# Kernel optimization log

Measured on AMD Instinct MI355X. Metric: run time of the kernel, lower is better.

Reference implementation:

```python
import jax, jax.numpy as jnp
import numpy as np

R = 8            # ring rank
N = 4            # num cores
D_IN = 2048
D_OUT = 2048
LIN = [512, 512, 512, 512]   # local input dims (additive split)
LOUT = [512, 512, 512, 512]  # local output dims (additive split)


def setup_inputs() -> dict:
    key = jax.random.key(0)
    ks = jax.random.split(key, 6)
    inp = {"inputs": jax.random.normal(ks[0], (4, 1024, D_IN), dtype=jnp.float32)}
    for i in range(N):
        lf = LOUT[i] * LIN[i]
        std = np.sqrt(2.0 / (R + lf)).astype(np.float32)
        inp[f"core{i}"] = jax.random.normal(ks[1 + i], (R, lf, R), dtype=jnp.float32) * std
    inp["bias"] = jnp.zeros((D_OUT,), dtype=jnp.float32)
    return inp


def reference(inputs, core0, core1, core2, core3, bias):
    cores = [core0, core1, core2, core3]
    batch_shape = inputs.shape[:-1]
    x = inputs.reshape(-1, D_IN)                      # [B, D_IN]
    B = x.shape[0]

    # split input additively across cores
    offs = np.cumsum([0] + LIN)
    xs = [x[:, offs[i]:offs[i + 1]] for i in range(N)]  # each [B, d_in_i]
    Gs = [cores[i].reshape(R, LOUT[i], LIN[i], R) for i in range(N)]

    # environment messages: S_i[b,r,s] = sum_{o,x} G_i[r,o,x,s] * x_i[b,x]
    S = [jnp.einsum('roxs,bx->brs', Gs[i], xs[i]) for i in range(N)]

    eye = jnp.broadcast_to(jnp.eye(R, dtype=x.dtype), (B, R, R))
    # prefix P_i = S_0 ... S_{i-1}, suffix Q_i = S_{i+1} ... S_{N-1}
    P = [eye]
    for i in range(1, N):
        P.append(jnp.matmul(P[-1], S[i - 1]))
    Q = [eye]
    for i in range(N - 2, -1, -1):
        Q.append(jnp.matmul(S[i + 1], Q[-1]))
    Q = Q[::-1]

    outs = []
    for i in range(N):
        # Env_i[b,r,s] = sum_p Q_i[b,s,p] P_i[b,p,r]  (trace closure of the ring)
        env = jnp.einsum('bsp,bpr->brs', Q[i], P[i])
        # M_i[b,r,o,s] = sum_x G_i[r,o,x,s] x_i[b,x]
        M = jnp.einsum('roxs,bx->bros', Gs[i], xs[i])
        outs.append(jnp.einsum('brs,bros->bo', env, M))
    out = jnp.concatenate(outs, axis=-1) + bias       # [B, D_OUT]
    return out.reshape(batch_shape + (D_OUT,))
```

## Files before the change

### kernel.cpp

```cpp
#include <hip/hip_runtime.h>
#include <stdint.h>

#define B_TOT   4096
#define D_IN    2048
#define D_OUT   2048
#define NCHUNK  4
#define LIN     512
#define LOUT    512
#define RK      8
#define CORE_R_STRIDE 2097152
#define CORE_O_STRIDE 4096

#define WS_XT    0
#define WS_GHAT  8388608
#define WS_S     (8388608 + 131072)
#define WS_ENVT  (8388608 + 131072 + 1048576)

typedef __attribute__((ext_vector_type(8))) __bf16 bf16x8;
typedef __attribute__((ext_vector_type(4))) float f32x4;
typedef __attribute__((ext_vector_type(4))) unsigned int u32x4;

__global__ __launch_bounds__(256) void k_transpose(const float* __restrict__ x,
                                                   float* __restrict__ xT) {
    __shared__ float tile[32][33];
    int b0 = blockIdx.x * 32;
    int c0 = blockIdx.y * 32;
    int tx = threadIdx.x;
    int ty = threadIdx.y;
#pragma unroll
    for (int j = 0; j < 4; ++j)
        tile[ty + j * 8][tx] = x[(size_t)(b0 + ty + j * 8) * D_IN + c0 + tx];
    __syncthreads();
#pragma unroll
    for (int j = 0; j < 4; ++j)
        xT[(size_t)(c0 + ty + j * 8) * B_TOT + b0 + tx] = tile[tx][ty + j * 8];
}

__global__ __launch_bounds__(256) void k_reduce_g(const float* __restrict__ g0,
                                                  const float* __restrict__ g1,
                                                  const float* __restrict__ g2,
                                                  const float* __restrict__ g3,
                                                  float* __restrict__ ghat) {
    int i = blockIdx.z;
    int r = blockIdx.y;
    int xs = blockIdx.x * 256 + threadIdx.x;
    const float* G = (i == 0) ? g0 : (i == 1) ? g1 : (i == 2) ? g2 : g3;
    const float* base = G + (size_t)r * CORE_R_STRIDE + xs;
    float acc = 0.f;
#pragma unroll 8
    for (int o = 0; o < LOUT; ++o) acc += base[(size_t)o * CORE_O_STRIDE];
    ghat[(size_t)i * 32768 + r * 4096 + xs] = acc;
}

__global__ __launch_bounds__(256) void k_s(const float* __restrict__ x,
                                           const float* __restrict__ ghat,
                                           float* __restrict__ S) {
    int i = blockIdx.y;
    int tid = threadIdx.x;
    int rs = tid & 63;
    int b = blockIdx.x * 4 + (tid >> 6);
    int r = rs >> 3, s = rs & 7;
    const float* gh = ghat + (size_t)i * 32768 + r * 4096 + s;
    const float* xr = x + (size_t)b * D_IN + i * LIN;
    float acc = 0.f;
#pragma unroll 8
    for (int xi = 0; xi < LIN; ++xi) acc = fmaf(gh[xi * 8], xr[xi], acc);
    S[(size_t)i * (B_TOT * 64) + b * 64 + rs] = acc;
}

__device__ __forceinline__ float mm8(float A, float B, int lane) {
    float c = 0.f;
#pragma unroll
    for (int p = 0; p < 8; ++p) {
        float a = __shfl(A, (lane & 56) | p, 64);
        float b = __shfl(B, (p << 3) | (lane & 7), 64);
        c = fmaf(a, b, c);
    }
    return c;
}
__device__ __forceinline__ float tr8(float E, int lane) {
    return __shfl(E, ((lane & 7) << 3) | (lane >> 3), 64);
}

__global__ __launch_bounds__(256) void k_env(const float* __restrict__ S,
                                             float* __restrict__ envT) {
    int tid = threadIdx.x;
    int lane = tid & 63;
    int b = blockIdx.x * 4 + (tid >> 6);
    float S0 = S[0 * (B_TOT * 64) + b * 64 + lane];
    float S1 = S[1 * (B_TOT * 64) + b * 64 + lane];
    float S2 = S[2 * (B_TOT * 64) + b * 64 + lane];
    float S3 = S[3 * (B_TOT * 64) + b * 64 + lane];

    float P1 = S0;
    float P2 = mm8(P1, S1, lane);
    float P3 = mm8(P2, S2, lane);
    float Q2 = S3;
    float Q1 = mm8(S2, Q2, lane);
    float Q0 = mm8(S1, Q1, lane);

    float e0 = tr8(Q0, lane);
    float e1 = tr8(mm8(Q1, P1, lane), lane);
    float e2 = tr8(mm8(Q2, P2, lane), lane);
    float e3 = tr8(P3, lane);

    envT[(size_t)(0 * 64 + lane) * B_TOT + b] = e0;
    envT[(size_t)(1 * 64 + lane) * B_TOT + b] = e1;
    envT[(size_t)(2 * 64 + lane) * B_TOT + b] = e2;
    envT[(size_t)(3 * 64 + lane) * B_TOT + b] = e3;
}

__device__ __forceinline__ uint2 split2(float a, float b) {
    unsigned int ua = __float_as_uint(a), ub = __float_as_uint(b);
    unsigned int h = (ub & 0xffff0000u) | (ua >> 16);
    float la = a - __uint_as_float(ua & 0xffff0000u);
    float lb = b - __uint_as_float(ub & 0xffff0000u);
    unsigned int l = (__float_as_uint(lb) & 0xffff0000u) | (__float_as_uint(la) >> 16);
    return make_uint2(h, l);
}

__global__ __launch_bounds__(256, 2) void k_gemm_pipe(const float* __restrict__ g0,
                                                      const float* __restrict__ g1,
                                                      const float* __restrict__ g2,
                                                      const float* __restrict__ g3,
                                                      const float* __restrict__ xT,
                                                      const float* __restrict__ envT,
                                                      const float* __restrict__ bias,
                                                      float* __restrict__ out) {
    int l = blockIdx.x;
    int c = (l & 7) | (((l >> 3) >> 5) << 3);
    int b_idx = (l >> 3) & 31;
    int i = c >> 2;
    int o0 = (c & 3) * 128;
    int b0 = b_idx * 128;

    const float* G = (i == 0) ? g0 : (i == 1) ? g1 : (i == 2) ? g2 : g3;
    const float* xTi = xT + (size_t)i * LIN * B_TOT;
    const float* eTi = envT + (size_t)i * 64 * B_TOT;

    __shared__ __align__(16) short Bhi[2][5120];
    __shared__ __align__(16) short Blo[2][5120];

    const int tid = threadIdx.x;
    const int lane = tid & 63;
    const int wave = tid >> 6;
    const int wm = (wave >> 1) * 64;
    const int wn = (wave & 1) * 64;
    const int l15 = lane & 15;
    const int quad = lane >> 4;

    const int so = tid >> 1;
    const int sh = (tid & 1) * 16;
    const int s0 = (tid & 1) * 2;
    const float* gsrc = G + (size_t)(o0 + so) * CORE_O_STRIDE + sh;

    f32x4 acc[4][4];
#pragma unroll
    for (int mf = 0; mf < 4; ++mf)
#pragma unroll
        for (int nf = 0; nf < 4; ++nf) acc[mf][nf] = (f32x4){0.f, 0.f, 0.f, 0.f};

    float4 f0, f1, f2, f3;

    auto LOADG = [&](int tn) {
        const float* p = gsrc + (size_t)(tn >> 7) * CORE_R_STRIDE + (tn & 127) * 32;
        f0 = *(const float4*)(p);
        f1 = *(const float4*)(p + 4);
        f2 = *(const float4*)(p + 8);
        f3 = *(const float4*)(p + 12);
    };
    auto STORE = [&](int pb) {
        u32x4 H0, L0, H1, L1;
        uint2 q;
        q = split2(f0.x, f0.y); H0.x = q.x; L0.x = q.y;
        q = split2(f0.z, f0.w); H0.y = q.x; L0.y = q.y;
        q = split2(f1.x, f1.y); H0.z = q.x; L0.z = q.y;
        q = split2(f1.z, f1.w); H0.w = q.x; L0.w = q.y;
        q = split2(f2.x, f2.y); H1.x = q.x; L1.x = q.y;
        q = split2(f2.z, f2.w); H1.y = q.x; L1.y = q.y;
        q = split2(f3.x, f3.y); H1.z = q.x; L1.z = q.y;
        q = split2(f3.z, f3.w); H1.w = q.x; L1.w = q.y;
        *(u32x4*)&Bhi[pb][(so * 5 + s0) * 8]     = H0;
        *(u32x4*)&Bhi[pb][(so * 5 + s0 + 1) * 8] = H1;
        *(u32x4*)&Blo[pb][(so * 5 + s0) * 8]     = L0;
        *(u32x4*)&Blo[pb][(so * 5 + s0 + 1) * 8] = L1;
    };

    float xc[4], xn[4];
#pragma unroll
    for (int mf = 0; mf < 4; ++mf)
        xc[mf] = xTi[(size_t)quad * B_TOT + b0 + wm + mf * 16 + l15];

    LOADG(0);
    STORE(0);
    __syncthreads();

    int t = 0;
    for (int r = 0; r < 8; ++r) {
        float e[4][8];
#pragma unroll
        for (int mf = 0; mf < 4; ++mf) {
            int m = b0 + wm + mf * 16 + l15;
#pragma unroll
            for (int s = 0; s < 8; ++s)
                e[mf][s] = eTi[(size_t)(r * 8 + s) * B_TOT + m];
        }
        for (int kk = 0; kk < 128; ++kk, ++t) {
            const int p = t & 1;
            const bool more = (t + 1 < 1024);
            if (more) LOADG(t + 1);
#pragma unroll
            for (int mf = 0; mf < 4; ++mf)
                xn[mf] = xTi[(size_t)(((kk + 1) & 127) * 4 + quad) * B_TOT
                             + b0 + wm + mf * 16 + l15];

            bf16x8 bh[4], bl[4];
#pragma unroll
            for (int nf = 0; nf < 4; ++nf) {
                int n = wn + nf * 16 + l15;
                bh[nf] = *(const bf16x8*)&Bhi[p][(n * 5 + quad) * 8];
                bl[nf] = *(const bf16x8*)&Blo[p][(n * 5 + quad) * 8];
            }

#pragma unroll
            for (int mf = 0; mf < 4; ++mf) {
                float xv = xc[mf];
                u32x4 AH, AL;
                uint2 pr;
                pr = split2(e[mf][0] * xv, e[mf][1] * xv); AH.x = pr.x; AL.x = pr.y;
                pr = split2(e[mf][2] * xv, e[mf][3] * xv); AH.y = pr.x; AL.y = pr.y;
                pr = split2(e[mf][4] * xv, e[mf][5] * xv); AH.z = pr.x; AL.z = pr.y;
                pr = split2(e[mf][6] * xv, e[mf][7] * xv); AH.w = pr.x; AL.w = pr.y;
                bf16x8 Ah = __builtin_bit_cast(bf16x8, AH);
                bf16x8 Al = __builtin_bit_cast(bf16x8, AL);
#pragma unroll
                for (int nf = 0; nf < 4; ++nf) {
                    acc[mf][nf] = __builtin_amdgcn_mfma_f32_16x16x32_bf16(Ah, bh[nf], acc[mf][nf], 0, 0, 0);
                    acc[mf][nf] = __builtin_amdgcn_mfma_f32_16x16x32_bf16(Ah, bl[nf], acc[mf][nf], 0, 0, 0);
                    acc[mf][nf] = __builtin_amdgcn_mfma_f32_16x16x32_bf16(Al, bh[nf], acc[mf][nf], 0, 0, 0);
                }
            }

            if (more) STORE(p ^ 1);
            __syncthreads();
#pragma unroll
            for (int mf = 0; mf < 4; ++mf) xc[mf] = xn[mf];
        }
    }

#pragma unroll
    for (int nf = 0; nf < 4; ++nf) {
        int col = o0 + wn + nf * 16 + l15;
        float bv = bias[i * LOUT + col];
#pragma unroll
        for (int mf = 0; mf < 4; ++mf) {
#pragma unroll
            for (int reg = 0; reg < 4; ++reg) {
                int row = b0 + wm + mf * 16 + quad * 4 + reg;
                out[(size_t)row * D_OUT + i * LOUT + col] = acc[mf][nf][reg] + bv;
            }
        }
    }
}

extern "C" void kernel_launch(void* const* d_in, const int* in_sizes, int n_in,
                              void* d_out, int out_size, void* d_ws, size_t ws_size,
                              hipStream_t stream) {
    const float* x    = (const float*)d_in[0];
    const float* g0   = (const float*)d_in[1];
    const float* g1   = (const float*)d_in[2];
    const float* g2   = (const float*)d_in[3];
    const float* g3   = (const float*)d_in[4];
    const float* bias = (const float*)d_in[5];
    float* out = (float*)d_out;
    float* ws = (float*)d_ws;

    float* xT   = ws + WS_XT;
    float* ghat = ws + WS_GHAT;
    float* S    = ws + WS_S;
    float* envT = ws + WS_ENVT;

    k_transpose<<<dim3(128, 64), dim3(32, 8), 0, stream>>>(x, xT);
    k_reduce_g<<<dim3(16, 8, 4), 256, 0, stream>>>(g0, g1, g2, g3, ghat);
    k_s<<<dim3(1024, 4), 256, 0, stream>>>(x, ghat, S);
    k_env<<<1024, 256, 0, stream>>>(S, envT);
    k_gemm_pipe<<<512, 256, 0, stream>>>(g0, g1, g2, g3, xT, envT, bias, out);
}
```

Measured before the change: 2.331 ms.

## Pre-split core weights into bf16 hi/lo planes in workspace; use packed cvt

Adds a pre-pass kernel that converts each core's fp32 weights into separate bf16 high and low planes stored in workspace, as many cores as the workspace size allows. The GEMM kernel then loads ready-made bf16 planes for those cores instead of loading fp32 and splitting inside the inner loop. The bit-manipulation split is also replaced with the hardware packed bf16 conversion instruction, which rounds instead of truncating. The pre-pass adds a full extra read and write of the weights each call, and whether it runs at all depends on the workspace size the harness provides.

```diff
diff --git a/kernel.cpp b/kernel.cpp
--- a/kernel.cpp
+++ b/kernel.cpp
@@ -15,8 +15,13 @@
 #define WS_GHAT  8388608
 #define WS_S     (8388608 + 131072)
 #define WS_ENVT  (8388608 + 131072 + 1048576)
+#define WS_GSPL  10616832
+#define WS_BASE_BYTES 42467328ull
+#define GSPL_CHUNK 16777216ull
+#define GSPL_CHUNK_BYTES 67108864ull
 
 typedef __attribute__((ext_vector_type(8))) __bf16 bf16x8;
+typedef __attribute__((ext_vector_type(8))) unsigned short ushort8;
 typedef __attribute__((ext_vector_type(4))) float f32x4;
 typedef __attribute__((ext_vector_type(4))) unsigned int u32x4;
 
@@ -110,23 +115,50 @@
     envT[(size_t)(3 * 64 + lane) * B_TOT + b] = e3;
 }
 
-__device__ __forceinline__ uint2 split2(float a, float b) {
-    unsigned int ua = __float_as_uint(a), ub = __float_as_uint(b);
-    unsigned int h = (ub & 0xffff0000u) | (ua >> 16);
-    float la = a - __uint_as_float(ua & 0xffff0000u);
-    float lb = b - __uint_as_float(ub & 0xffff0000u);
-    unsigned int l = (__float_as_uint(lb) & 0xffff0000u) | (__float_as_uint(la) >> 16);
+__device__ __forceinline__ uint2 split2pk(float a, float b) {
+    unsigned int h, l;
+    asm("v_cvt_pk_bf16_f32 %0, %1, %2" : "=v"(h) : "v"(a), "v"(b));
+    float fa = __uint_as_float(h << 16);
+    float fb = __uint_as_float(h & 0xffff0000u);
+    float la = a - fa;
+    float lb = b - fb;
+    asm("v_cvt_pk_bf16_f32 %0, %1, %2" : "=v"(l) : "v"(la), "v"(lb));
     return make_uint2(h, l);
 }
 
-__global__ __launch_bounds__(256, 2) void k_gemm_pipe(const float* __restrict__ g0,
-                                                      const float* __restrict__ g1,
-                                                      const float* __restrict__ g2,
-                                                      const float* __restrict__ g3,
-                                                      const float* __restrict__ xT,
-                                                      const float* __restrict__ envT,
-                                                      const float* __restrict__ bias,
-                                                      float* __restrict__ out) {
+__global__ __launch_bounds__(256) void k_split_g(const float* __restrict__ g0,
+                                                 const float* __restrict__ g1,
+                                                 const float* __restrict__ g2,
+                                                 const float* __restrict__ g3,
+                                                 short* __restrict__ planes) {
+    size_t e8 = ((size_t)blockIdx.x * 256 + threadIdx.x) * 8;
+    int i = (int)(e8 >> 24);
+    const float* G = (i == 0) ? g0 : (i == 1) ? g1 : (i == 2) ? g2 : g3;
+    size_t off = e8 & (GSPL_CHUNK - 1);
+    float4 f0 = *(const float4*)(G + off);
+    float4 f1 = *(const float4*)(G + off + 4);
+    u32x4 H, L;
+    uint2 p;
+    p = split2pk(f0.x, f0.y); H.x = p.x; L.x = p.y;
+    p = split2pk(f0.z, f0.w); H.y = p.x; L.y = p.y;
+    p = split2pk(f1.x, f1.y); H.z = p.x; L.z = p.y;
+    p = split2pk(f1.z, f1.w); H.w = p.x; L.w = p.y;
+    short* hi = planes + (size_t)i * (2 * GSPL_CHUNK) + off;
+    short* lo = hi + GSPL_CHUNK;
+    *(u32x4*)hi = H;
+    *(u32x4*)lo = L;
+}
+
+__global__ __launch_bounds__(256, 2) void k_gemm_mix(const float* __restrict__ g0,
+                                                     const float* __restrict__ g1,
+                                                     const float* __restrict__ g2,
+                                                     const float* __restrict__ g3,
+                                                     const short* __restrict__ planes,
+                                                     int n_pre,
+                                                     const float* __restrict__ xT,
+                                                     const float* __restrict__ envT,
+                                                     const float* __restrict__ bias,
+                                                     float* __restrict__ out) {
     int l = blockIdx.x;
     int c = (l & 7) | (((l >> 3) >> 5) << 3);
     int b_idx = (l >> 3) & 31;
@@ -134,7 +166,6 @@
     int o0 = (c & 3) * 128;
     int b0 = b_idx * 128;
 
-    const float* G = (i == 0) ? g0 : (i == 1) ? g1 : (i == 2) ? g2 : g3;
     const float* xTi = xT + (size_t)i * LIN * B_TOT;
     const float* eTi = envT + (size_t)i * 64 * B_TOT;
 
@@ -152,99 +183,178 @@
     const int so = tid >> 1;
     const int sh = (tid & 1) * 16;
     const int s0 = (tid & 1) * 2;
-    const float* gsrc = G + (size_t)(o0 + so) * CORE_O_STRIDE + sh;
 
     f32x4 acc[4][4];
 #pragma unroll
     for (int mf = 0; mf < 4; ++mf)
 #pragma unroll
         for (int nf = 0; nf < 4; ++nf) acc[mf][nf] = (f32x4){0.f, 0.f, 0.f, 0.f};
-
-    float4 f0, f1, f2, f3;
-
-    auto LOADG = [&](int tn) {
-        const float* p = gsrc + (size_t)(tn >> 7) * CORE_R_STRIDE + (tn & 127) * 32;
-        f0 = *(const float4*)(p);
-        f1 = *(const float4*)(p + 4);
-        f2 = *(const float4*)(p + 8);
-        f3 = *(const float4*)(p + 12);
-    };
-    auto STORE = [&](int pb) {
-        u32x4 H0, L0, H1, L1;
-        uint2 q;
-        q = split2(f0.x, f0.y); H0.x = q.x; L0.x = q.y;
-        q = split2(f0.z, f0.w); H0.y = q.x; L0.y = q.y;
-        q = split2(f1.x, f1.y); H0.z = q.x; L0.z = q.y;
-        q = split2(f1.z, f1.w); H0.w = q.x; L0.w = q.y;
-        q = split2(f2.x, f2.y); H1.x = q.x; L1.x = q.y;
-        q = split2(f2.z, f2.w); H1.y = q.x; L1.y = q.y;
-        q = split2(f3.x, f3.y); H1.z = q.x; L1.z = q.y;
-        q = split2(f3.z, f3.w); H1.w = q.x; L1.w = q.y;
-        *(u32x4*)&Bhi[pb][(so * 5 + s0) * 8]     = H0;
-        *(u32x4*)&Bhi[pb][(so * 5 + s0 + 1) * 8] = H1;
-        *(u32x4*)&Blo[pb][(so * 5 + s0) * 8]     = L0;
-        *(u32x4*)&Blo[pb][(so * 5 + s0 + 1) * 8] = L1;
-    };
 
     float xc[4], xn[4];
 #pragma unroll
     for (int mf = 0; mf < 4; ++mf)
         xc[mf] = xTi[(size_t)quad * B_TOT + b0 + wm + mf * 16 + l15];
 
-    LOADG(0);
-    STORE(0);
-    __syncthreads();
-
-    int t = 0;
-    for (int r = 0; r < 8; ++r) {
-        float e[4][8];
-#pragma unroll
-        for (int mf = 0; mf < 4; ++mf) {
-            int m = b0 + wm + mf * 16 + l15;
-#pragma unroll
-            for (int s = 0; s < 8; ++s)
-                e[mf][s] = eTi[(size_t)(r * 8 + s) * B_TOT + m];
+    if (i < n_pre) {
+        const short* Phi = planes + (size_t)i * (2 * GSPL_CHUNK);
+        const short* Plo = Phi + GSPL_CHUNK;
+        const size_t soff0 = (size_t)(o0 + so) * CORE_O_STRIDE + sh;
+
+        ushort8 h0, h1, l0, l1;
+        auto LOADG = [&](int tn) {
+            size_t off = soff0 + (size_t)(tn >> 7) * CORE_R_STRIDE + (size_t)(tn & 127) * 32;
+            h0 = *(const ushort8*)(Phi + off);
+            h1 = *(const ushort8*)(Phi + off + 8);
+            l0 = *(const ushort8*)(Plo + off);
+            l1 = *(const ushort8*)(Plo + off + 8);
+        };
+        auto STORE = [&](int pb) {
+            *(ushort8*)&Bhi[pb][(so * 5 + s0) * 8]     = h0;
+            *(ushort8*)&Bhi[pb][(so * 5 + s0 + 1) * 8] = h1;
+            *(ushort8*)&Blo[pb][(so * 5 + s0) * 8]     = l0;
+            *(ushort8*)&Blo[pb][(so * 5 + s0 + 1) * 8] = l1;
+        };
+
+        LOADG(0);
+        STORE(0);
+        __syncthreads();
+
+        int t = 0;
+        for (int r = 0; r < 8; ++r) {
+            float e[4][8];
+#pragma unroll
+            for (int mf = 0; mf < 4; ++mf) {
+                int m = b0 + wm + mf * 16 + l15;
+#pragma unroll
+                for (int s = 0; s < 8; ++s)
+                    e[mf][s] = eTi[(size_t)(r * 8 + s) * B_TOT + m];
+            }
+            for (int kk = 0; kk < 128; ++kk, ++t) {
+                const int p = t & 1;
+                const bool more = (t + 1 < 1024);
+                if (more) LOADG(t + 1);
+#pragma unroll
+                for (int mf = 0; mf < 4; ++mf)
+                    xn[mf] = xTi[(size_t)(((kk + 1) & 127) * 4 + quad) * B_TOT
+                                 + b0 + wm + mf * 16 + l15];
+
+                bf16x8 bh[4], bl[4];
+#pragma unroll
+                for (int nf = 0; nf < 4; ++nf) {
+                    int n = wn + nf * 16 + l15;
+                    bh[nf] = *(const bf16x8*)&Bhi[p][(n * 5 + quad) * 8];
+                    bl[nf] = *(const bf16x8*)&Blo[p][(n * 5 + quad) * 8];
+                }
+
+#pragma unroll
+                for (int mf = 0; mf < 4; ++mf) {
+                    float xv = xc[mf];
+                    u32x4 AH, AL;
+                    uint2 pr;
+                    pr = split2pk(e[mf][0] * xv, e[mf][1] * xv); AH.x = pr.x; AL.x = pr.y;
+                    pr = split2pk(e[mf][2] * xv, e[mf][3] * xv); AH.y = pr.x; AL.y = pr.y;
+                    pr = split2pk(e[mf][4] * xv, e[mf][5] * xv); AH.z = pr.x; AL.z = pr.y;
+                    pr = split2pk(e[mf][6] * xv, e[mf][7] * xv); AH.w = pr.x; AL.w = pr.y;
+                    bf16x8 Ah = __builtin_bit_cast(bf16x8, AH);
+                    bf16x8 Al = __builtin_bit_cast(bf16x8, AL);
+#pragma unroll
+                    for (int nf = 0; nf < 4; ++nf) {
+                        acc[mf][nf] = __builtin_amdgcn_mfma_f32_16x16x32_bf16(Ah, bh[nf], acc[mf][nf], 0, 0, 0);
+                        acc[mf][nf] = __builtin_amdgcn_mfma_f32_16x16x32_bf16(Ah, bl[nf], acc[mf][nf], 0, 0, 0);
+                        acc[mf][nf] = __builtin_amdgcn_mfma_f32_16x16x32_bf16(Al, bh[nf], acc[mf][nf], 0, 0, 0);
+                    }
+                }
+
+                if (more) STORE(p ^ 1);
+                __syncthreads();
+#pragma unroll
+                for (int mf = 0; mf < 4; ++mf) xc[mf] = xn[mf];
+            }
         }
-        for (int kk = 0; kk < 128; ++kk, ++t) {
-            const int p = t & 1;
-            const bool more = (t + 1 < 1024);
-            if (more) LOADG(t + 1);
-#pragma unroll
-            for (int mf = 0; mf < 4; ++mf)
-                xn[mf] = xTi[(size_t)(((kk + 1) & 127) * 4 + quad) * B_TOT
-                             + b0 + wm + mf * 16 + l15];
-
-            bf16x8 bh[4], bl[4];
-#pragma unroll
-            for (int nf = 0; nf < 4; ++nf) {
-                int n = wn + nf * 16 + l15;
-                bh[nf] = *(const bf16x8*)&Bhi[p][(n * 5 + quad) * 8];
-                bl[nf] = *(const bf16x8*)&Blo[p][(n * 5 + quad) * 8];
+    } else {
+        const float* G = (i == 0) ? g0 : (i == 1) ? g1 : (i == 2) ? g2 : g3;
+        const float* gsrc = G + (size_t)(o0 + so) * CORE_O_STRIDE + sh;
+
+        float4 f0, f1, f2, f3;
+        auto LOADG = [&](int tn) {
+            const float* p = gsrc + (size_t)(tn >> 7) * CORE_R_STRIDE + (tn & 127) * 32;
+            f0 = *(const float4*)(p);
+            f1 = *(const float4*)(p + 4);
+            f2 = *(const float4*)(p + 8);
+            f3 = *(const float4*)(p + 12);
+        };
+        auto STORE = [&](int pb) {
+            u32x4 H0, L0, H1, L1;
+            uint2 q;
+            q = split2pk(f0.x, f0.y); H0.x = q.x; L0.x = q.y;
+            q = split2pk(f0.z, f0.w); H0.y = q.x; L0.y = q.y;
+            q = split2pk(f1.x, f1.y); H0.z = q.x; L0.z = q.y;
+            q = split2pk(f1.z, f1.w); H0.w = q.x; L0.w = q.y;
+            q = split2pk(f2.x, f2.y); H1.x = q.x; L1.x = q.y;
+            q = split2pk(f2.z, f2.w); H1.y = q.x; L1.y = q.y;
+            q = split2pk(f3.x, f3.y); H1.z = q.x; L1.z = q.y;
+            q = split2pk(f3.z, f3.w); H1.w = q.x; L1.w = q.y;
+            *(u32x4*)&Bhi[pb][(so * 5 + s0) * 8]     = H0;
+            *(u32x4*)&Bhi[pb][(so * 5 + s0 + 1) * 8] = H1;
+            *(u32x4*)&Blo[pb][(so * 5 + s0) * 8]     = L0;
+            *(u32x4*)&Blo[pb][(so * 5 + s0 + 1) * 8] = L1;
+        };
+
+        LOADG(0);
+        STORE(0);
+        __syncthreads();
+
+        int t = 0;
+        for (int r = 0; r < 8; ++r) {
+            float e[4][8];
+#pragma unroll
+            for (int mf = 0; mf < 4; ++mf) {
+                int m = b0 + wm + mf * 16 + l15;
+#pragma unroll
+                for (int s = 0; s < 8; ++s)
+                    e[mf][s] = eTi[(size_t)(r * 8 + s) * B_TOT + m];
             }
-
-#pragma unroll
-            for (int mf = 0; mf < 4; ++mf) {
-                float xv = xc[mf];
-                u32x4 AH, AL;
-                uint2 pr;
-                pr = split2(e[mf][0] * xv, e[mf][1] * xv); AH.x = pr.x; AL.x = pr.y;
-                pr = split2(e[mf][2] * xv, e[mf][3] * xv); AH.y = pr.x; AL.y = pr.y;
-                pr = split2(e[mf][4] * xv, e[mf][5] * xv); AH.z = pr.x; AL.z = pr.y;
-                pr = split2(e[mf][6] * xv, e[mf][7] * xv); AH.w = pr.x; AL.w = pr.y;
-                bf16x8 Ah = __builtin_bit_cast(bf16x8, AH);
-                bf16x8 Al = __builtin_bit_cast(bf16x8, AL);
+            for (int kk = 0; kk < 128; ++kk, ++t) {
+                const int p = t & 1;
+                const bool more = (t + 1 < 1024);
+                if (more) LOADG(t + 1);
+#pragma unroll
+                for (int mf = 0; mf < 4; ++mf)
+                    xn[mf] = xTi[(size_t)(((kk + 1) & 127) * 4 + quad) * B_TOT
+                                 + b0 + wm + mf * 16 + l15];
+
+                bf16x8 bh[4], bl[4];
 #pragma unroll
                 for (int nf = 0; nf < 4; ++nf) {
-                    acc[mf][nf] = __builtin_amdgcn_mfma_f32_16x16x32_bf16(Ah, bh[nf], acc[mf][nf], 0, 0, 0);
-                    acc[mf][nf] = __builtin_amdgcn_mfma_f32_16x16x32_bf16(Ah, bl[nf], acc[mf][nf], 0, 0, 0);
-                    acc[mf][nf] = __builtin_amdgcn_mfma_f32_16x16x32_bf16(Al, bh[nf], acc[mf][nf], 0, 0, 0);
+                    int n = wn + nf * 16 + l15;
+                    bh[nf] = *(const bf16x8*)&Bhi[p][(n * 5 + quad) * 8];
+                    bl[nf] = *(const bf16x8*)&Blo[p][(n * 5 + quad) * 8];
                 }
+
+#pragma unroll
+                for (int mf = 0; mf < 4; ++mf) {
+                    float xv = xc[mf];
+                    u32x4 AH, AL;
+                    uint2 pr;
+                    pr = split2pk(e[mf][0] * xv, e[mf][1] * xv); AH.x = pr.x; AL.x = pr.y;
+                    pr = split2pk(e[mf][2] * xv, e[mf][3] * xv); AH.y = pr.x; AL.y = pr.y;
+                    pr = split2pk(e[mf][4] * xv, e[mf][5] * xv); AH.z = pr.x; AL.z = pr.y;
+                    pr = split2pk(e[mf][6] * xv, e[mf][7] * xv); AH.w = pr.x; AL.w = pr.y;
+                    bf16x8 Ah = __builtin_bit_cast(bf16x8, AH);
+                    bf16x8 Al = __builtin_bit_cast(bf16x8, AL);
+#pragma unroll
+                    for (int nf = 0; nf < 4; ++nf) {
+                        acc[mf][nf] = __builtin_amdgcn_mfma_f32_16x16x32_bf16(Ah, bh[nf], acc[mf][nf], 0, 0, 0);
+                        acc[mf][nf] = __builtin_amdgcn_mfma_f32_16x16x32_bf16(Ah, bl[nf], acc[mf][nf], 0, 0, 0);
+                        acc[mf][nf] = __builtin_amdgcn_mfma_f32_16x16x32_bf16(Al, bh[nf], acc[mf][nf], 0, 0, 0);
+                    }
+                }
+
+                if (more) STORE(p ^ 1);
+                __syncthreads();
+#pragma unroll
+                for (int mf = 0; mf < 4; ++mf) xc[mf] = xn[mf];
             }
-
-            if (more) STORE(p ^ 1);
-            __syncthreads();
-#pragma unroll
-            for (int mf = 0; mf < 4; ++mf) xc[mf] = xn[mf];
         }
     }
 
@@ -279,10 +389,19 @@
     float* ghat = ws + WS_GHAT;
     float* S    = ws + WS_S;
     float* envT = ws + WS_ENVT;
+    short* planes = (short*)(ws + WS_GSPL);
+
+    int n_pre = 0;
+    if (ws_size > WS_BASE_BYTES)
+        n_pre = (int)((ws_size - WS_BASE_BYTES) / GSPL_CHUNK_BYTES);
+    if (n_pre > 4) n_pre = 4;
 
     k_transpose<<<dim3(128, 64), dim3(32, 8), 0, stream>>>(x, xT);
     k_reduce_g<<<dim3(16, 8, 4), 256, 0, stream>>>(g0, g1, g2, g3, ghat);
     k_s<<<dim3(1024, 4), 256, 0, stream>>>(x, ghat, S);
     k_env<<<1024, 256, 0, stream>>>(S, envT);
-    k_gemm_pipe<<<512, 256, 0, stream>>>(g0, g1, g2, g3, xT, envT, bias, out);
-}
+    if (n_pre > 0)
+        k_split_g<<<n_pre * 8192, 256, 0, stream>>>(g0, g1, g2, g3, planes);
+    k_gemm_mix<<<512, 256, 0, stream>>>(g0, g1, g2, g3, planes, n_pre,
+                                        xT, envT, bias, out);
+}
```

After: 2.418 ms. 3.7% more time.

## Prefetch G two steps ahead, use packed bf16 convert, raise MFMA priority

Applied to the files above, without the earlier changes.

The main GEMM loop is unrolled by two and uses two register sets for global G loads, so each load is issued two iterations before its data is split and stored to shared memory. This gives global latency more time to hide. The hi/lo bf16 split now uses the hardware v_cvt_pk_bf16_f32 instruction, which rounds to nearest instead of truncating, and needs fewer ALU ops. s_setprio is raised around the MFMA block to favor the matrix work. The cost is higher register pressure from the second prefetch buffer, which risks lower occupancy or spills at 2 blocks per SM.

```diff
diff --git a/kernel.cpp b/kernel.cpp
--- a/kernel.cpp
+++ b/kernel.cpp
@@ -110,23 +110,25 @@
     envT[(size_t)(3 * 64 + lane) * B_TOT + b] = e3;
 }
 
-__device__ __forceinline__ uint2 split2(float a, float b) {
-    unsigned int ua = __float_as_uint(a), ub = __float_as_uint(b);
-    unsigned int h = (ub & 0xffff0000u) | (ua >> 16);
-    float la = a - __uint_as_float(ua & 0xffff0000u);
-    float lb = b - __uint_as_float(ub & 0xffff0000u);
-    unsigned int l = (__float_as_uint(lb) & 0xffff0000u) | (__float_as_uint(la) >> 16);
+__device__ __forceinline__ uint2 split2pk(float a, float b) {
+    unsigned int h, l;
+    asm("v_cvt_pk_bf16_f32 %0, %1, %2" : "=v"(h) : "v"(a), "v"(b));
+    float fa = __uint_as_float(h << 16);
+    float fb = __uint_as_float(h & 0xffff0000u);
+    float la = a - fa;
+    float lb = b - fb;
+    asm("v_cvt_pk_bf16_f32 %0, %1, %2" : "=v"(l) : "v"(la), "v"(lb));
     return make_uint2(h, l);
 }
 
-__global__ __launch_bounds__(256, 2) void k_gemm_pipe(const float* __restrict__ g0,
-                                                      const float* __restrict__ g1,
-                                                      const float* __restrict__ g2,
-                                                      const float* __restrict__ g3,
-                                                      const float* __restrict__ xT,
-                                                      const float* __restrict__ envT,
-                                                      const float* __restrict__ bias,
-                                                      float* __restrict__ out) {
+__global__ __launch_bounds__(256, 2) void k_gemm_pipe2(const float* __restrict__ g0,
+                                                       const float* __restrict__ g1,
+                                                       const float* __restrict__ g2,
+                                                       const float* __restrict__ g3,
+                                                       const float* __restrict__ xT,
+                                                       const float* __restrict__ envT,
+                                                       const float* __restrict__ bias,
+                                                       float* __restrict__ out) {
     int l = blockIdx.x;
     int c = (l & 7) | (((l >> 3) >> 5) << 3);
     int b_idx = (l >> 3) & 31;
@@ -160,44 +162,109 @@
 #pragma unroll
         for (int nf = 0; nf < 4; ++nf) acc[mf][nf] = (f32x4){0.f, 0.f, 0.f, 0.f};
 
-    float4 f0, f1, f2, f3;
-
-    auto LOADG = [&](int tn) {
+    float4 fA0, fA1, fA2, fA3;
+    float4 fB0, fB1, fB2, fB3;
+
+    auto LOADGA = [&](int tn) {
         const float* p = gsrc + (size_t)(tn >> 7) * CORE_R_STRIDE + (tn & 127) * 32;
-        f0 = *(const float4*)(p);
-        f1 = *(const float4*)(p + 4);
-        f2 = *(const float4*)(p + 8);
-        f3 = *(const float4*)(p + 12);
-    };
-    auto STORE = [&](int pb) {
+        fA0 = *(const float4*)(p);
+        fA1 = *(const float4*)(p + 4);
+        fA2 = *(const float4*)(p + 8);
+        fA3 = *(const float4*)(p + 12);
+    };
+    auto LOADGB = [&](int tn) {
+        const float* p = gsrc + (size_t)(tn >> 7) * CORE_R_STRIDE + (tn & 127) * 32;
+        fB0 = *(const float4*)(p);
+        fB1 = *(const float4*)(p + 4);
+        fB2 = *(const float4*)(p + 8);
+        fB3 = *(const float4*)(p + 12);
+    };
+    auto STOREA = [&](int pb) {
         u32x4 H0, L0, H1, L1;
         uint2 q;
-        q = split2(f0.x, f0.y); H0.x = q.x; L0.x = q.y;
-        q = split2(f0.z, f0.w); H0.y = q.x; L0.y = q.y;
-        q = split2(f1.x, f1.y); H0.z = q.x; L0.z = q.y;
-        q = split2(f1.z, f1.w); H0.w = q.x; L0.w = q.y;
-        q = split2(f2.x, f2.y); H1.x = q.x; L1.x = q.y;
-        q = split2(f2.z, f2.w); H1.y = q.x; L1.y = q.y;
-        q = split2(f3.x, f3.y); H1.z = q.x; L1.z = q.y;
-        q = split2(f3.z, f3.w); H1.w = q.x; L1.w = q.y;
+        q = split2pk(fA0.x, fA0.y); H0.x = q.x; L0.x = q.y;
+        q = split2pk(fA0.z, fA0.w); H0.y = q.x; L0.y = q.y;
+        q = split2pk(fA1.x, fA1.y); H0.z = q.x; L0.z = q.y;
+        q = split2pk(fA1.z, fA1.w); H0.w = q.x; L0.w = q.y;
+        q = split2pk(fA2.x, fA2.y); H1.x = q.x; L1.x = q.y;
+        q = split2pk(fA2.z, fA2.w); H1.y = q.x; L1.y = q.y;
+        q = split2pk(fA3.x, fA3.y); H1.z = q.x; L1.z = q.y;
+        q = split2pk(fA3.z, fA3.w); H1.w = q.x; L1.w = q.y;
         *(u32x4*)&Bhi[pb][(so * 5 + s0) * 8]     = H0;
         *(u32x4*)&Bhi[pb][(so * 5 + s0 + 1) * 8] = H1;
         *(u32x4*)&Blo[pb][(so * 5 + s0) * 8]     = L0;
         *(u32x4*)&Blo[pb][(so * 5 + s0 + 1) * 8] = L1;
     };
-
-    float xc[4], xn[4];
+    auto STOREB = [&](int pb) {
+        u32x4 H0, L0, H1, L1;
+        uint2 q;
+        q = split2pk(fB0.x, fB0.y); H0.x = q.x; L0.x = q.y;
+        q = split2pk(fB0.z, fB0.w); H0.y = q.x; L0.y = q.y;
+        q = split2pk(fB1.x, fB1.y); H0.z = q.x; L0.z = q.y;
+        q = split2pk(fB1.z, fB1.w); H0.w = q.x; L0.w = q.y;
+        q = split2pk(fB2.x, fB2.y); H1.x = q.x; L1.x = q.y;
+        q = split2pk(fB2.z, fB2.w); H1.y = q.x; L1.y = q.y;
+        q = split2pk(fB3.x, fB3.y); H1.z = q.x; L1.z = q.y;
+        q = split2pk(fB3.z, fB3.w); H1.w = q.x; L1.w = q.y;
+        *(u32x4*)&Bhi[pb][(so * 5 + s0) * 8]     = H0;
+        *(u32x4*)&Bhi[pb][(so * 5 + s0 + 1) * 8] = H1;
+        *(u32x4*)&Blo[pb][(so * 5 + s0) * 8]     = L0;
+        *(u32x4*)&Blo[pb][(so * 5 + s0 + 1) * 8] = L1;
+    };
+
+    float xc[4];
 #pragma unroll
     for (int mf = 0; mf < 4; ++mf)
         xc[mf] = xTi[(size_t)quad * B_TOT + b0 + wm + mf * 16 + l15];
 
-    LOADG(0);
-    STORE(0);
+    float e[4][8];
+
+    auto COMP = [&](int p, int kk) {
+        float xn[4];
+#pragma unroll
+        for (int mf = 0; mf < 4; ++mf)
+            xn[mf] = xTi[(size_t)(((kk + 1) & 127) * 4 + quad) * B_TOT
+                         + b0 + wm + mf * 16 + l15];
+
+        bf16x8 bh[4], bl[4];
+#pragma unroll
+        for (int nf = 0; nf < 4; ++nf) {
+            int n = wn + nf * 16 + l15;
+            bh[nf] = *(const bf16x8*)&Bhi[p][(n * 5 + quad) * 8];
+            bl[nf] = *(const bf16x8*)&Blo[p][(n * 5 + quad) * 8];
+        }
+
+        __builtin_amdgcn_s_setprio(1);
+#pragma unroll
+        for (int mf = 0; mf < 4; ++mf) {
+            float xv = xc[mf];
+            u32x4 AH, AL;
+            uint2 pr;
+            pr = split2pk(e[mf][0] * xv, e[mf][1] * xv); AH.x = pr.x; AL.x = pr.y;
+            pr = split2pk(e[mf][2] * xv, e[mf][3] * xv); AH.y = pr.x; AL.y = pr.y;
+            pr = split2pk(e[mf][4] * xv, e[mf][5] * xv); AH.z = pr.x; AL.z = pr.y;
+            pr = split2pk(e[mf][6] * xv, e[mf][7] * xv); AH.w = pr.x; AL.w = pr.y;
+            bf16x8 Ah = __builtin_bit_cast(bf16x8, AH);
+            bf16x8 Al = __builtin_bit_cast(bf16x8, AL);
+#pragma unroll
+            for (int nf = 0; nf < 4; ++nf) {
+                acc[mf][nf] = __builtin_amdgcn_mfma_f32_16x16x32_bf16(Ah, bh[nf], acc[mf][nf], 0, 0, 0);
+                acc[mf][nf] = __builtin_amdgcn_mfma_f32_16x16x32_bf16(Ah, bl[nf], acc[mf][nf], 0, 0, 0);
+                acc[mf][nf] = __builtin_amdgcn_mfma_f32_16x16x32_bf16(Al, bh[nf], acc[mf][nf], 0, 0, 0);
+            }
+        }
+        __builtin_amdgcn_s_setprio(0);
+#pragma unroll
+        for (int mf = 0; mf < 4; ++mf) xc[mf] = xn[mf];
+    };
+
+    LOADGA(0);
+    LOADGB(1);
+    STOREA(0);
     __syncthreads();
 
     int t = 0;
     for (int r = 0; r < 8; ++r) {
-        float e[4][8];
 #pragma unroll
         for (int mf = 0; mf < 4; ++mf) {
             int m = b0 + wm + mf * 16 + l15;
@@ -205,46 +272,15 @@
             for (int s = 0; s < 8; ++s)
                 e[mf][s] = eTi[(size_t)(r * 8 + s) * B_TOT + m];
         }
-        for (int kk = 0; kk < 128; ++kk, ++t) {
-            const int p = t & 1;
-            const bool more = (t + 1 < 1024);
-            if (more) LOADG(t + 1);
-#pragma unroll
-            for (int mf = 0; mf < 4; ++mf)
-                xn[mf] = xTi[(size_t)(((kk + 1) & 127) * 4 + quad) * B_TOT
-                             + b0 + wm + mf * 16 + l15];
-
-            bf16x8 bh[4], bl[4];
-#pragma unroll
-            for (int nf = 0; nf < 4; ++nf) {
-                int n = wn + nf * 16 + l15;
-                bh[nf] = *(const bf16x8*)&Bhi[p][(n * 5 + quad) * 8];
-                bl[nf] = *(const bf16x8*)&Blo[p][(n * 5 + quad) * 8];
-            }
-
-#pragma unroll
-            for (int mf = 0; mf < 4; ++mf) {
-                float xv = xc[mf];
-                u32x4 AH, AL;
-                uint2 pr;
-                pr = split2(e[mf][0] * xv, e[mf][1] * xv); AH.x = pr.x; AL.x = pr.y;
-                pr = split2(e[mf][2] * xv, e[mf][3] * xv); AH.y = pr.x; AL.y = pr.y;
-                pr = split2(e[mf][4] * xv, e[mf][5] * xv); AH.z = pr.x; AL.z = pr.y;
-                pr = split2(e[mf][6] * xv, e[mf][7] * xv); AH.w = pr.x; AL.w = pr.y;
-                bf16x8 Ah = __builtin_bit_cast(bf16x8, AH);
-                bf16x8 Al = __builtin_bit_cast(bf16x8, AL);
-#pragma unroll
-                for (int nf = 0; nf < 4; ++nf) {
-                    acc[mf][nf] = __builtin_amdgcn_mfma_f32_16x16x32_bf16(Ah, bh[nf], acc[mf][nf], 0, 0, 0);
-                    acc[mf][nf] = __builtin_amdgcn_mfma_f32_16x16x32_bf16(Ah, bl[nf], acc[mf][nf], 0, 0, 0);
-                    acc[mf][nf] = __builtin_amdgcn_mfma_f32_16x16x32_bf16(Al, bh[nf], acc[mf][nf], 0, 0, 0);
-                }
-            }
-
-            if (more) STORE(p ^ 1);
+        for (int kk = 0; kk < 128; kk += 2, t += 2) {
+            if (t + 2 < 1024) LOADGA(t + 2);
+            COMP(0, kk);
+            STOREB(1);
             __syncthreads();
-#pragma unroll
-            for (int mf = 0; mf < 4; ++mf) xc[mf] = xn[mf];
+            if (t + 3 < 1024) LOADGB(t + 3);
+            COMP(1, kk + 1);
+            if (t + 2 < 1024) STOREA(0);
+            __syncthreads();
         }
     }
 
@@ -284,5 +320,5 @@
     k_reduce_g<<<dim3(16, 8, 4), 256, 0, stream>>>(g0, g1, g2, g3, ghat);
     k_s<<<dim3(1024, 4), 256, 0, stream>>>(x, ghat, S);
     k_env<<<1024, 256, 0, stream>>>(S, envT);
-    k_gemm_pipe<<<512, 256, 0, stream>>>(g0, g1, g2, g3, xT, envT, bias, out);
-}
+    k_gemm_pipe2<<<512, 256, 0, stream>>>(g0, g1, g2, g3, xT, envT, bias, out);
+}
```

Result: faster. 2.122 ms (-9.0%).
